# Kernel tuning notes

Hardware: AMD Instinct MI355X
Metric: run time of the kernel (lower is better)

The kernel has to match this reference:

```python
import jax, jax.numpy as jnp
import numpy as np

B = 16
SR = 16000
DUR = 3
L = SR * DUR          # 48000 samples
W = 64                # n_wavetables
LWT = 512             # wavetable_len


def setup_inputs() -> dict:
    key = jax.random.key(0)
    k1, k2, k3, k4 = jax.random.split(key, 4)
    # Per-sample F0 in a realistic range (CREPE-style, upsampled to sr)
    pitch = jax.random.uniform(k1, (B, L), dtype=jnp.float32, minval=50.0, maxval=500.0)
    envelope = jax.random.uniform(k2, (B, L, 1), dtype=jnp.float32)
    # attention is "already softmaxed" per the docstring
    attention = jax.nn.softmax(jax.random.normal(k3, (B, L, W), dtype=jnp.float32), axis=-1)
    # Wavetable bank: first 4 are fixed sines with cycles 1..4, rest N(0, 0.01)
    i = jnp.arange(LWT, dtype=jnp.float32)
    fixed = jnp.stack([jnp.sin(c * 2.0 * jnp.pi * i / LWT) for c in (1, 2, 3, 4)], axis=0)
    learned = 0.01 * jax.random.normal(k4, (W - 4, LWT), dtype=jnp.float32)
    wavetables = jnp.concatenate([fixed, learned], axis=0)  # [W, LWT]
    return {"pitch": pitch, "envelope": envelope, "attention": attention, "wavetables": wavetables}


def reference(pitch, envelope, attention, wavetables):
    lwt = wavetables.shape[1]
    # phase increment per sample, per batch item: [B, L]
    increment = (lwt / SR) * pitch
    # NOTE: faithful to original torch code: subtracts the FIRST BATCH ROW
    # of increments (broadcast over batch), not a per-row first element.
    index = jnp.cumsum(increment, axis=1) - increment[0]
    index = jnp.remainder(index, lwt)
    index = jnp.where(lwt - index < 1e-05, 0.0, index)
    low = jnp.floor(index)
    alpha = index - low                       # [B, L]
    idx_low = low.astype(jnp.int32)           # in [0, lwt-1]
    idx_high = jnp.ceil(index).astype(jnp.int32) % lwt
    # Dual gather across all 64 wavetables at once: [W, B, L]
    wl = wavetables[:, idx_low]
    wh = wavetables[:, idx_high]
    waves = wl + alpha[None, :, :] * (wh - wl)  # linear interpolation
    # attention-weighted sum over wavetables, then envelope: [B, L, 1]
    out = jnp.einsum('wbl,blw->bl', waves, attention)[..., None] * envelope
    return out
```

## Files before the change

kernel.cpp:

```cpp
#include <hip/hip_runtime.h>
#include <hip/hip_fp16.h>

#define BB    16
#define LL    48000
#define WW    64
#define LWT   512
#define CHUNK 750
#define NCH   64
#define NELEM (BB*LL)
#define NGRP  (NELEM/4)
#define RATIO (512.0/16000.0)

#define KD_THREADS 512
#define KD_BLOCKS  512
#define KD_WAVES   (KD_BLOCKS * (KD_THREADS/64))
#define GPW        ((NGRP + KD_WAVES - 1) / KD_WAVES)

__global__ void kA(const float* __restrict__ pitch, double* __restrict__ csum,
                   const float* __restrict__ wt, __half* __restrict__ tab) {
    int bid = blockIdx.x;
    if (bid >= BB * NCH) {
        int tid = (bid - BB * NCH) * 256 + threadIdx.x;
        int idx = tid >> 6, w = tid & 63;
        tab[tid] = __float2half(wt[w * LWT + idx]);
        return;
    }
    int r = bid >> 6, c = bid & 63;
    int t = threadIdx.x;
    double s = 0.0;
    if (t < 250) {
        const float* p = pitch + r * LL + c * CHUNK + t * 3;
        s = RATIO * (double)p[0] + RATIO * (double)p[1] + RATIO * (double)p[2];
    }
    for (int d = 1; d < 64; d <<= 1) s += __shfl_xor(s, d);
    __shared__ double wsh[4];
    if ((t & 63) == 0) wsh[t >> 6] = s;
    __syncthreads();
    if (t == 0) csum[bid] = wsh[0] + wsh[1] + wsh[2] + wsh[3];
}

__global__ void kB(const double* __restrict__ csum, double* __restrict__ cbase) {
    int r = threadIdx.x >> 6, c = threadIdx.x & 63;
    double v = csum[r * NCH + c];
    double inc = v;
    for (int d = 1; d < 64; d <<= 1) {
        double u = __shfl_up(inc, d);
        if (c >= d) inc += u;
    }
    cbase[r * NCH + c] = inc - v;
}

__global__ void kC(const float* __restrict__ pitch,
                   const double* __restrict__ cbase,
                   unsigned* __restrict__ packed) {
    int bid = blockIdx.x;
    int r = bid >> 6, c = bid & 63;
    int t = threadIdx.x;
    int lane = t & 63, wv = t >> 6;
    int l = c * CHUNK + t * 3;
    bool act = (t < 250);
    double i0 = 0.0, i1 = 0.0, i2 = 0.0;
    if (act) {
        const float* p = pitch + r * LL + l;
        i0 = RATIO * (double)p[0];
        i1 = RATIO * (double)p[1];
        i2 = RATIO * (double)p[2];
    }
    double c0 = i0, c1 = i0 + i1, c2 = c1 + i2;
    double inc = c2;
    for (int d = 1; d < 64; d <<= 1) {
        double u = __shfl_up(inc, d);
        if (lane >= d) inc += u;
    }
    __shared__ double wsum[4];
    if (lane == 63) wsum[wv] = inc;
    __syncthreads();
    double wb = 0.0;
    for (int i = 0; i < wv; i++) wb += wsum[i];
    if (!act) return;
    double base = cbase[bid] + (wb + inc - c2);
    double pre[3] = {c0, c1, c2};
    for (int k = 0; k < 3; k++) {
        double inc0 = RATIO * (double)pitch[l + k];
        double idx = base + pre[k] - inc0;
        double m = idx - floor(idx * (1.0 / 512.0)) * 512.0;
        if (m < 0.0) m += 512.0;
        if (512.0 - m < 1e-5) m = 0.0;
        double lowd = floor(m);
        double alpha = m - lowd;
        unsigned il = (unsigned)lowd;
        unsigned au = (unsigned)(alpha * 8388608.0 + 0.5);
        if (au > 0x7fffffu) au = 0x7fffffu;
        packed[r * LL + l + k] = (il << 23) | au;
    }
}

__global__ __launch_bounds__(KD_THREADS) void kD(const float4* __restrict__ attn4,
                                                 const float* __restrict__ env,
                                                 const unsigned* __restrict__ packed,
                                                 const __half* __restrict__ tabG,
                                                 float* __restrict__ out) {
    __shared__ __half tab[LWT * WW];
    {
        const uint4* s4 = (const uint4*)tabG;
        uint4* d4 = (uint4*)tab;
        for (int i = threadIdx.x; i < (LWT * WW) / 8; i += KD_THREADS) d4[i] = s4[i];
    }
    __syncthreads();
    const int lane = threadIdx.x & 63;
    const int sub = lane >> 4;
    const int li  = lane & 15;
    const int wid = (blockIdx.x << 3) | (threadIdx.x >> 6);
    int g0 = wid * GPW;
    int g1 = g0 + GPW;
    if (g1 > NGRP) g1 = NGRP;
    if (g0 >= g1) return;

    float4  a0 = attn4[(size_t)g0 * 64 + lane];
    unsigned p0 = packed[(g0 << 2) | sub];
    float4  a1 = a0;
    unsigned p1 = p0;
    if (g0 + 1 < g1) {
        a1 = attn4[(size_t)(g0 + 1) * 64 + lane];
        p1 = packed[((g0 + 1) << 2) | sub];
    }
    for (int g = g0; g < g1; ++g) {
        float4 ac = a0;
        unsigned pc = p0;
        a0 = a1; p0 = p1;
        int gn = g + 2;
        if (gn < g1) {
            a1 = attn4[(size_t)gn * 64 + lane];
            p1 = packed[(gn << 2) | sub];
        }
        unsigned il = pc >> 23;
        float alpha = (float)(pc & 0x7fffffu) * (1.0f / 8388608.0f);
        unsigned ih = (il + 1) & 511;
        uint2 lo = *(const uint2*)(tab + (il << 6) + (li << 2));
        uint2 hi = *(const uint2*)(tab + (ih << 6) + (li << 2));
        __half2 l01 = *(__half2*)&lo.x, l23 = *(__half2*)&lo.y;
        __half2 h01 = *(__half2*)&hi.x, h23 = *(__half2*)&hi.y;
        float2 fl01 = __half22float2(l01), fl23 = __half22float2(l23);
        float2 fh01 = __half22float2(h01), fh23 = __half22float2(h23);
        float w0 = fmaf(alpha, fh01.x - fl01.x, fl01.x);
        float w1 = fmaf(alpha, fh01.y - fl01.y, fl01.y);
        float w2 = fmaf(alpha, fh23.x - fl23.x, fl23.x);
        float w3 = fmaf(alpha, fh23.y - fl23.y, fl23.y);
        float s = w0 * ac.x + w1 * ac.y + w2 * ac.z + w3 * ac.w;
        s += __shfl_xor(s, 1);
        s += __shfl_xor(s, 2);
        s += __shfl_xor(s, 4);
        s += __shfl_xor(s, 8);
        if (li == 0) {
            int e = (g << 2) | sub;
            out[e] = s * env[e];
        }
    }
}

extern "C" void kernel_launch(void* const* d_in, const int* in_sizes, int n_in,
                              void* d_out, int out_size, void* d_ws, size_t ws_size,
                              hipStream_t stream) {
    const float* pitch = (const float*)d_in[0];
    const float* env   = (const float*)d_in[1];
    const float* attn  = (const float*)d_in[2];
    const float* wt    = (const float*)d_in[3];
    float* out = (float*)d_out;

    char* ws = (char*)d_ws;
    __half*   tab    = (__half*)(ws);
    double*   csum   = (double*)(ws + 65536);
    double*   cbase  = (double*)(ws + 73728);
    unsigned* packed = (unsigned*)(ws + 81920);

    kA<<<BB * NCH + 128, 256, 0, stream>>>(pitch, csum, wt, tab);
    kB<<<1, 1024, 0, stream>>>(csum, cbase);
    kC<<<BB * NCH, 256, 0, stream>>>(pitch, cbase, packed);
    kD<<<KD_BLOCKS, KD_THREADS, 0, stream>>>((const float4*)attn, env, packed, tab, out);
}
```

Measured before the change: 292.4 us.

## Merge three-kernel prefix scan into one per-row kernel and deepen kD prefetch

Replaces the chunk-sum, chunk-scan and index-pack kernels with a single kScan kernel. It runs one 1024-thread block per batch row, and each thread serially accumulates and writes 47 consecutive samples. This removes two kernel launches and the intermediate csum/cbase buffers. The cost is that only 16 blocks do the scan work, and the per-thread strided loads are poorly coalesced. Separately, the main kD loop's software prefetch of attention and packed indices goes from two to three groups ahead.

```diff
diff --git a/kernel.cpp b/kernel.cpp
--- a/kernel.cpp
+++ b/kernel.cpp
@@ -5,8 +5,6 @@
 #define LL    48000
 #define WW    64
 #define LWT   512
-#define CHUNK 750
-#define NCH   64
 #define NELEM (BB*LL)
 #define NGRP  (NELEM/4)
 #define RATIO (512.0/16000.0)
@@ -16,73 +14,54 @@
 #define KD_WAVES   (KD_BLOCKS * (KD_THREADS/64))
 #define GPW        ((NGRP + KD_WAVES - 1) / KD_WAVES)
 
-__global__ void kA(const float* __restrict__ pitch, double* __restrict__ csum,
-                   const float* __restrict__ wt, __half* __restrict__ tab) {
+#define EPT 47
+
+__global__ __launch_bounds__(1024) void kScan(const float* __restrict__ pitch,
+                                              const float* __restrict__ wt,
+                                              __half* __restrict__ tab,
+                                              unsigned* __restrict__ packed) {
     int bid = blockIdx.x;
-    if (bid >= BB * NCH) {
-        int tid = (bid - BB * NCH) * 256 + threadIdx.x;
-        int idx = tid >> 6, w = tid & 63;
-        tab[tid] = __float2half(wt[w * LWT + idx]);
+    int t = threadIdx.x;
+    if (bid >= BB) {
+        int base = (bid - BB) * 16384;
+        #pragma unroll
+        for (int i = 0; i < 16; i++) {
+            int tid2 = base + i * 1024 + t;
+            int idx = tid2 >> 6, w = tid2 & 63;
+            tab[tid2] = __float2half(wt[w * LWT + idx]);
+        }
         return;
     }
-    int r = bid >> 6, c = bid & 63;
-    int t = threadIdx.x;
+    const int r = bid;
+    const int lane = t & 63, wv = t >> 6;
+    int l0 = t * EPT;
+    int l1 = l0 + EPT; if (l1 > LL) l1 = LL;
+    bool act = (l0 < LL);
+
     double s = 0.0;
-    if (t < 250) {
-        const float* p = pitch + r * LL + c * CHUNK + t * 3;
-        s = RATIO * (double)p[0] + RATIO * (double)p[1] + RATIO * (double)p[2];
+    if (act) {
+        const float* p = pitch + (size_t)r * LL;
+        for (int j = l0; j < l1; j++) s += RATIO * (double)p[j];
     }
-    for (int d = 1; d < 64; d <<= 1) s += __shfl_xor(s, d);
-    __shared__ double wsh[4];
-    if ((t & 63) == 0) wsh[t >> 6] = s;
-    __syncthreads();
-    if (t == 0) csum[bid] = wsh[0] + wsh[1] + wsh[2] + wsh[3];
-}
-
-__global__ void kB(const double* __restrict__ csum, double* __restrict__ cbase) {
-    int r = threadIdx.x >> 6, c = threadIdx.x & 63;
-    double v = csum[r * NCH + c];
-    double inc = v;
-    for (int d = 1; d < 64; d <<= 1) {
-        double u = __shfl_up(inc, d);
-        if (c >= d) inc += u;
-    }
-    cbase[r * NCH + c] = inc - v;
-}
-
-__global__ void kC(const float* __restrict__ pitch,
-                   const double* __restrict__ cbase,
-                   unsigned* __restrict__ packed) {
-    int bid = blockIdx.x;
-    int r = bid >> 6, c = bid & 63;
-    int t = threadIdx.x;
-    int lane = t & 63, wv = t >> 6;
-    int l = c * CHUNK + t * 3;
-    bool act = (t < 250);
-    double i0 = 0.0, i1 = 0.0, i2 = 0.0;
-    if (act) {
-        const float* p = pitch + r * LL + l;
-        i0 = RATIO * (double)p[0];
-        i1 = RATIO * (double)p[1];
-        i2 = RATIO * (double)p[2];
-    }
-    double c0 = i0, c1 = i0 + i1, c2 = c1 + i2;
-    double inc = c2;
+    double inc = s;
     for (int d = 1; d < 64; d <<= 1) {
         double u = __shfl_up(inc, d);
         if (lane >= d) inc += u;
     }
-    __shared__ double wsum[4];
+    __shared__ double wsum[16];
     if (lane == 63) wsum[wv] = inc;
     __syncthreads();
     double wb = 0.0;
     for (int i = 0; i < wv; i++) wb += wsum[i];
     if (!act) return;
-    double base = cbase[bid] + (wb + inc - c2);
-    double pre[3] = {c0, c1, c2};
-    for (int k = 0; k < 3; k++) {
-        double inc0 = RATIO * (double)pitch[l + k];
-        double idx = base + pre[k] - inc0;
+    double running = wb + inc - s;
+
+    const float* prow = pitch + (size_t)r * LL;
+    unsigned* orow = packed + (size_t)r * LL;
+    for (int j = l0; j < l1; j++) {
+        running += RATIO * (double)prow[j];
+        double inc0 = RATIO * (double)pitch[j];
+        double idx = running - inc0;
         double m = idx - floor(idx * (1.0 / 512.0)) * 512.0;
         if (m < 0.0) m += 512.0;
         if (512.0 - m < 1e-5) m = 0.0;
@@ -91,7 +70,7 @@
         unsigned il = (unsigned)lowd;
         unsigned au = (unsigned)(alpha * 8388608.0 + 0.5);
         if (au > 0x7fffffu) au = 0x7fffffu;
-        packed[r * LL + l + k] = (il << 23) | au;
+        orow[j] = (il << 23) | au;
     }
 }
 
@@ -115,23 +94,26 @@
     int g1 = g0 + GPW;
     if (g1 > NGRP) g1 = NGRP;
     if (g0 >= g1) return;
+    const int gl = g1 - 1;
 
     float4  a0 = attn4[(size_t)g0 * 64 + lane];
     unsigned p0 = packed[(g0 << 2) | sub];
-    float4  a1 = a0;
-    unsigned p1 = p0;
-    if (g0 + 1 < g1) {
-        a1 = attn4[(size_t)(g0 + 1) * 64 + lane];
-        p1 = packed[((g0 + 1) << 2) | sub];
-    }
+    int ga = g0 + 1 <= gl ? g0 + 1 : gl;
+    int gb = g0 + 2 <= gl ? g0 + 2 : gl;
+    float4  a1 = attn4[(size_t)ga * 64 + lane];
+    unsigned p1 = packed[(ga << 2) | sub];
+    float4  a2 = attn4[(size_t)gb * 64 + lane];
+    unsigned p2 = packed[(gb << 2) | sub];
+
     for (int g = g0; g < g1; ++g) {
         float4 ac = a0;
         unsigned pc = p0;
-        a0 = a1; p0 = p1;
-        int gn = g + 2;
-        if (gn < g1) {
-            a1 = attn4[(size_t)gn * 64 + lane];
-            p1 = packed[(gn << 2) | sub];
+        a0 = a1; a1 = a2;
+        p0 = p1; p1 = p2;
+        int gn = g + 3;
+        if (gn <= gl) {
+            a2 = attn4[(size_t)gn * 64 + lane];
+            p2 = packed[(gn << 2) | sub];
         }
         unsigned il = pc >> 23;
         float alpha = (float)(pc & 0x7fffffu) * (1.0f / 8388608.0f);
@@ -161,6 +143,7 @@
 extern "C" void kernel_launch(void* const* d_in, const int* in_sizes, int n_in,
                               void* d_out, int out_size, void* d_ws, size_t ws_size,
                               hipStream_t stream) {
+    (void)in_sizes; (void)n_in; (void)out_size; (void)ws_size;
     const float* pitch = (const float*)d_in[0];
     const float* env   = (const float*)d_in[1];
     const float* attn  = (const float*)d_in[2];
@@ -169,12 +152,8 @@
 
     char* ws = (char*)d_ws;
     __half*   tab    = (__half*)(ws);
-    double*   csum   = (double*)(ws + 65536);
-    double*   cbase  = (double*)(ws + 73728);
-    unsigned* packed = (unsigned*)(ws + 81920);
+    unsigned* packed = (unsigned*)(ws + 65536);
 
-    kA<<<BB * NCH + 128, 256, 0, stream>>>(pitch, csum, wt, tab);
-    kB<<<1, 1024, 0, stream>>>(csum, cbase);
-    kC<<<BB * NCH, 256, 0, stream>>>(pitch, cbase, packed);
+    kScan<<<BB + 2, 1024, 0, stream>>>(pitch, wt, tab, packed);
     kD<<<KD_BLOCKS, KD_THREADS, 0, stream>>>((const float4*)attn, env, packed, tab, out);
 }
```

Measured after the change: 425.3 us. 45.5% more time.

## Fold chunk-base scan into kC and deepen kD prefetch to three groups

Applied to the files above, without the earlier changes.

Removes the separate single-block scan kernel and has each kC block compute its chunk base by reducing the preceding chunk sums from csum in its first wave. This drops one kernel launch and its dependency hop. kD's software prefetch is also extended from two to three groups ahead, with clamped indices instead of conditional initial loads. The deeper prefetch raises register pressure a little, and every kC block now does redundant reduction work.

```diff
diff --git a/kernel.cpp b/kernel.cpp
--- a/kernel.cpp
+++ b/kernel.cpp
@@ -39,19 +39,8 @@
     if (t == 0) csum[bid] = wsh[0] + wsh[1] + wsh[2] + wsh[3];
 }
 
-__global__ void kB(const double* __restrict__ csum, double* __restrict__ cbase) {
-    int r = threadIdx.x >> 6, c = threadIdx.x & 63;
-    double v = csum[r * NCH + c];
-    double inc = v;
-    for (int d = 1; d < 64; d <<= 1) {
-        double u = __shfl_up(inc, d);
-        if (c >= d) inc += u;
-    }
-    cbase[r * NCH + c] = inc - v;
-}
-
 __global__ void kC(const float* __restrict__ pitch,
-                   const double* __restrict__ cbase,
+                   const double* __restrict__ csum,
                    unsigned* __restrict__ packed) {
     int bid = blockIdx.x;
     int r = bid >> 6, c = bid & 63;
@@ -73,12 +62,18 @@
         if (lane >= d) inc += u;
     }
     __shared__ double wsum[4];
+    __shared__ double cbs;
     if (lane == 63) wsum[wv] = inc;
+    if (wv == 0) {
+        double v = (lane < c) ? csum[(bid & ~63) + lane] : 0.0;
+        for (int d = 1; d < 64; d <<= 1) v += __shfl_xor(v, d);
+        if (lane == 0) cbs = v;
+    }
     __syncthreads();
     double wb = 0.0;
     for (int i = 0; i < wv; i++) wb += wsum[i];
     if (!act) return;
-    double base = cbase[bid] + (wb + inc - c2);
+    double base = cbs + (wb + inc - c2);
     double pre[3] = {c0, c1, c2};
     for (int k = 0; k < 3; k++) {
         double inc0 = RATIO * (double)pitch[l + k];
@@ -115,23 +110,26 @@
     int g1 = g0 + GPW;
     if (g1 > NGRP) g1 = NGRP;
     if (g0 >= g1) return;
+    const int gl = g1 - 1;
 
     float4  a0 = attn4[(size_t)g0 * 64 + lane];
     unsigned p0 = packed[(g0 << 2) | sub];
-    float4  a1 = a0;
-    unsigned p1 = p0;
-    if (g0 + 1 < g1) {
-        a1 = attn4[(size_t)(g0 + 1) * 64 + lane];
-        p1 = packed[((g0 + 1) << 2) | sub];
-    }
+    int ga = g0 + 1 <= gl ? g0 + 1 : gl;
+    int gb = g0 + 2 <= gl ? g0 + 2 : gl;
+    float4  a1 = attn4[(size_t)ga * 64 + lane];
+    unsigned p1 = packed[(ga << 2) | sub];
+    float4  a2 = attn4[(size_t)gb * 64 + lane];
+    unsigned p2 = packed[(gb << 2) | sub];
+
     for (int g = g0; g < g1; ++g) {
         float4 ac = a0;
         unsigned pc = p0;
-        a0 = a1; p0 = p1;
-        int gn = g + 2;
-        if (gn < g1) {
-            a1 = attn4[(size_t)gn * 64 + lane];
-            p1 = packed[(gn << 2) | sub];
+        a0 = a1; a1 = a2;
+        p0 = p1; p1 = p2;
+        int gn = g + 3;
+        if (gn <= gl) {
+            a2 = attn4[(size_t)gn * 64 + lane];
+            p2 = packed[(gn << 2) | sub];
         }
         unsigned il = pc >> 23;
         float alpha = (float)(pc & 0x7fffffu) * (1.0f / 8388608.0f);
@@ -161,6 +159,7 @@
 extern "C" void kernel_launch(void* const* d_in, const int* in_sizes, int n_in,
                               void* d_out, int out_size, void* d_ws, size_t ws_size,
                               hipStream_t stream) {
+    (void)in_sizes; (void)n_in; (void)out_size; (void)ws_size;
     const float* pitch = (const float*)d_in[0];
     const float* env   = (const float*)d_in[1];
     const float* attn  = (const float*)d_in[2];
@@ -170,11 +169,9 @@
     char* ws = (char*)d_ws;
     __half*   tab    = (__half*)(ws);
     double*   csum   = (double*)(ws + 65536);
-    double*   cbase  = (double*)(ws + 73728);
-    unsigned* packed = (unsigned*)(ws + 81920);
+    unsigned* packed = (unsigned*)(ws + 73728);
 
     kA<<<BB * NCH + 128, 256, 0, stream>>>(pitch, csum, wt, tab);
-    kB<<<1, 1024, 0, stream>>>(csum, cbase);
-    kC<<<BB * NCH, 256, 0, stream>>>(pitch, cbase, packed);
+    kC<<<BB * NCH, 256, 0, stream>>>(pitch, csum, packed);
     kD<<<KD_BLOCKS, KD_THREADS, 0, stream>>>((const float4*)attn, env, packed, tab, out);
 }
```

New measurement: 290.3 us. About the same (-0.7%).
